# Kernel tuning notes

Hardware: AMD Instinct MI355X
Metric: run time of the kernel (lower is better)

Reference implementation:

```python
import jax, jax.numpy as jnp
import numpy as np

N = 100000      # nodes
E = 1600000     # edges (avg degree 16)
IN = 256        # in_dim
OUT = 64        # out_dim per head
H = 4           # num_heads
SLOPE = 0.01    # F.leaky_relu default negative_slope


def setup_inputs() -> dict:
    key = jax.random.key(0)
    k1, k2, k3, k4, k5 = jax.random.split(key, 5)
    h = jax.random.normal(k1, (N, IN), dtype=jnp.float32)
    # per-head projection Linear(in_dim, out_dim, bias=False): weight [OUT, IN]
    W = jax.random.normal(k2, (H, OUT, IN), dtype=jnp.float32) * (1.0 / np.sqrt(IN))
    # per-head attention Linear(2*out_dim, 1, bias=False): weight flattened to [2*OUT]
    attn = jax.random.normal(k3, (H, 2 * OUT), dtype=jnp.float32) * (1.0 / np.sqrt(2 * OUT))
    edge_src = jax.random.randint(k4, (E,), 0, N, dtype=jnp.int32)
    edge_dst = jax.random.randint(k5, (E,), 0, N, dtype=jnp.int32)
    return {"h": h, "W": W, "attn": attn, "edge_src": edge_src, "edge_dst": edge_dst}


def reference(h, W, attn, edge_src, edge_dst):
    # Bug-faithful: edge_attention always uses self.heads[0][1], i.e. head 0's
    # attention vector, for every head.
    a0 = attn[0]                      # [2*OUT]
    a_src, a_dst = a0[:OUT], a0[OUT:]
    outs = []
    for hd in range(H):               # fixed small structural loop over heads
        z = h @ W[hd].T               # [N, OUT]
        # concat(z_src, z_dst) @ a0 == z_src @ a_src + z_dst @ a_dst
        s_src = z @ a_src             # [N]
        s_dst = z @ a_dst             # [N]
        e = jax.nn.leaky_relu(s_src[edge_src] + s_dst[edge_dst], SLOPE)  # [E]
        # segment softmax over incoming edges of each destination node
        m = jax.ops.segment_max(e, edge_dst, num_segments=N)
        m = jnp.where(jnp.isfinite(m), m, 0.0)   # guard zero-in-degree nodes
        ex = jnp.exp(e - m[edge_dst])
        den = jax.ops.segment_sum(ex, edge_dst, num_segments=N)
        alpha = ex / jnp.maximum(den[edge_dst], 1e-9)          # [E]
        msg = alpha[:, None] * z[edge_src]                      # [E, OUT]
        outs.append(jax.ops.segment_sum(msg, edge_dst, num_segments=N))  # [N, OUT]
    return jnp.concatenate(outs, axis=1)  # merge='cat' -> [N, H*OUT]
```

## Files before the change

kernel.cpp:

```cpp
#include <hip/hip_runtime.h>

#define K_IN   256
#define C_OUT  256
#define HEADS  4
#define PAD    64
#define BKT    256
#define REP    16
#define CAP    448

typedef __attribute__((ext_vector_type(8))) short s16x8;
typedef __attribute__((ext_vector_type(4))) short s16x4;
typedef __attribute__((ext_vector_type(4))) float f32x4;
typedef __attribute__((ext_vector_type(4))) int   i32x4;

static __device__ __forceinline__ unsigned short f2bf(float f) {
  union { float f; unsigned u; } v; v.f = f;
  unsigned r = v.u + 0x7FFFu + ((v.u >> 16) & 1u);
  return (unsigned short)(r >> 16);
}
static __device__ __forceinline__ float bf2f(unsigned short u) {
  union { unsigned u; float f; } v; v.u = (unsigned)u << 16;
  return v.f;
}
static __device__ __forceinline__ unsigned cvt_pk_bf16(float lo, float hi) {
  unsigned r;
  asm volatile("v_cvt_pk_bf16_f32 %0, %1, %2" : "=v"(r) : "v"(lo), "v"(hi));
  return r;
}
static __device__ __forceinline__ float fast_exp2(float x) {
  float r;
  asm("v_exp_f32 %0, %1" : "=v"(r) : "v"(x));
  return r;
}

__global__ void cvt_w(const float* __restrict__ Wm, unsigned short* __restrict__ Wf) {
  int idx = blockIdx.x * blockDim.x + threadIdx.x;
  if (idx >= 65536) return;
  int j    = idx & 7;
  int lane = (idx >> 3) & 63;
  int s    = (idx >> 9) & 3;
  int ks   = (idx >> 11) & 7;
  int cb   = (idx >> 14) & 3;
  int c = cb * 64 + s * 16 + (lane & 15);
  int k = ks * 32 + (lane >> 4) * 8 + j;
  Wf[idx] = f2bf(Wm[c * K_IN + k]);
}

__global__ __launch_bounds__(256) void gemm_z(const float* __restrict__ h,
                                              const unsigned short* __restrict__ Wf,
                                              const float* __restrict__ attn,
                                              unsigned short* __restrict__ zb,
                                              float* __restrict__ ssrc,
                                              float* __restrict__ sdst, int n_nodes) {
  const int wv   = threadIdx.x >> 6;
  const int lane = threadIdx.x & 63;
  const int l15  = lane & 15;
  const int lhi  = lane >> 4;
  const int r0   = blockIdx.x * 64 + wv * 16;

  f32x4 acc[16];
#pragma unroll
  for (int f = 0; f < 16; ++f) acc[f] = (f32x4){0.f, 0.f, 0.f, 0.f};

  int n = r0 + l15;
  if (n > n_nodes - 1) n = n_nodes - 1;
  const long long arow = (long long)n * K_IN;
  const int kbase = lhi * 8;

#pragma unroll
  for (int ks = 0; ks < 8; ++ks) {
    const int k = ks * 32 + kbase;
    const float4* pa = reinterpret_cast<const float4*>(h + arow + k);
    float4 v0 = pa[0], v1 = pa[1];
    union { s16x8 v; unsigned u[4]; } au;
    au.u[0] = cvt_pk_bf16(v0.x, v0.y);
    au.u[1] = cvt_pk_bf16(v0.z, v0.w);
    au.u[2] = cvt_pk_bf16(v1.x, v1.y);
    au.u[3] = cvt_pk_bf16(v1.z, v1.w);
    s16x8 a = au.v;
#pragma unroll
    for (int f = 0; f < 16; ++f) {
      s16x8 b = *reinterpret_cast<const s16x8*>(
          Wf + (((f >> 2) * 8 + ks) * 4 + (f & 3)) * 512 + lane * 8);
      acc[f] = __builtin_amdgcn_mfma_f32_16x16x32_bf16(a, b, acc[f], 0, 0, 0);
    }
  }

#pragma unroll
  for (int reg = 0; reg < 4; ++reg) {
    int row = r0 + lhi * 4 + reg;
    if (row < n_nodes) {
#pragma unroll
      for (int f = 0; f < 16; ++f)
        zb[(size_t)row * C_OUT + f * 16 + l15] = f2bf(acc[f][reg]);
    }
  }

  const float LOG2E = 1.4426950408889634f;
  float as_[4], ad_[4];
#pragma unroll
  for (int s = 0; s < 4; ++s) {
    as_[s] = attn[s * 16 + l15];
    ad_[s] = attn[64 + s * 16 + l15];
  }
#pragma unroll
  for (int reg = 0; reg < 4; ++reg) {
    int row = r0 + lhi * 4 + reg;
    float ps[4], pd[4];
#pragma unroll
    for (int hd = 0; hd < 4; ++hd) {
      ps[hd] = acc[hd * 4 + 0][reg] * as_[0] + acc[hd * 4 + 1][reg] * as_[1] +
               acc[hd * 4 + 2][reg] * as_[2] + acc[hd * 4 + 3][reg] * as_[3];
      pd[hd] = acc[hd * 4 + 0][reg] * ad_[0] + acc[hd * 4 + 1][reg] * ad_[1] +
               acc[hd * 4 + 2][reg] * ad_[2] + acc[hd * 4 + 3][reg] * ad_[3];
#pragma unroll
      for (int d = 1; d < 16; d <<= 1) {
        ps[hd] += __shfl_xor(ps[hd], d, 64);
        pd[hd] += __shfl_xor(pd[hd], d, 64);
      }
    }
    if (l15 == 0 && row < n_nodes) {
#pragma unroll
      for (int hd = 0; hd < 4; ++hd) {
        ssrc[(size_t)row * 4 + hd] = ps[hd] * LOG2E;
        sdst[(size_t)row * 4 + hd] = pd[hd] * LOG2E;
      }
    }
  }
}

__global__ void scatter_r1(const int* __restrict__ src, const int* __restrict__ dst,
                           int E, int* __restrict__ cursors, int* __restrict__ stage) {
  int i = blockIdx.x * blockDim.x + threadIdx.x;
  int rep = blockIdx.x & (REP - 1);
  int e4 = E >> 2;
  if (i < e4) {
    i32x4 d = __builtin_nontemporal_load(reinterpret_cast<const i32x4*>(dst) + i);
    i32x4 s = __builtin_nontemporal_load(reinterpret_cast<const i32x4*>(src) + i);
#pragma unroll
    for (int k = 0; k < 4; ++k) {
      int c = (d[k] >> 8) * REP + rep;
      int p = atomicAdd(&cursors[c], 1);
      if (p < CAP) stage[c * CAP + p] = (s[k] << 8) | (d[k] & 255);
    }
  }
  if (i < (E & 3)) {
    int j = (e4 << 2) + i;
    int dd = dst[j], ss = src[j];
    int c = (dd >> 8) * REP + rep;
    int p = atomicAdd(&cursors[c], 1);
    if (p < CAP) stage[c * CAP + p] = (ss << 8) | (dd & 255);
  }
}

__global__ __launch_bounds__(256) void scatter_r2(const int* __restrict__ cursors,
                                                  const int* __restrict__ stage,
                                                  int N, int* __restrict__ counts,
                                                  int* __restrict__ csrp) {
  int b = blockIdx.x;
  int base = b << 8;
  __shared__ int cnt[BKT];
  for (int i = threadIdx.x; i < BKT; i += 256) cnt[i] = 0;
  __syncthreads();
  for (int rep = 0; rep < REP; ++rep) {
    int c = b * REP + rep;
    int len = min(cursors[c], CAP);
    for (int j = threadIdx.x; j < len; j += 256) {
      int v = stage[c * CAP + j];
      int d = v & 255, s = v >> 8;
      int slot = atomicAdd(&cnt[d], 1);
      if (slot < PAD) csrp[(size_t)(base + d) * PAD + slot] = s;
    }
  }
  __syncthreads();
  for (int i = threadIdx.x; i < BKT; i += 256) {
    int n = base + i;
    if (n < N) counts[n] = min(cnt[i], PAD);
  }
}

__global__ void scatter_pad(const int* __restrict__ src, const int* __restrict__ dst,
                            int e, int* __restrict__ cursor, int* __restrict__ csrp) {
  int i = blockIdx.x * blockDim.x + threadIdx.x;
  int e4 = e >> 2;
  if (i < e4) {
    i32x4 d = __builtin_nontemporal_load(reinterpret_cast<const i32x4*>(dst) + i);
    i32x4 s = __builtin_nontemporal_load(reinterpret_cast<const i32x4*>(src) + i);
#pragma unroll
    for (int k = 0; k < 4; ++k) {
      int p = atomicAdd(&cursor[d[k]], 1);
      csrp[d[k] * PAD + p] = s[k];
    }
  }
  if (i < (e & 3)) {
    int j = (e4 << 2) + i;
    int p = atomicAdd(&cursor[dst[j]], 1);
    csrp[dst[j] * PAD + p] = src[j];
  }
}

__global__ __launch_bounds__(256) void aggregate(const unsigned short* __restrict__ zb,
                                                 const float* __restrict__ ssrc,
                                                 const float* __restrict__ sdst,
                                                 const int* __restrict__ cnts,
                                                 const int* __restrict__ csr,
                                                 float* __restrict__ out,
                                                 int n0, int n1) {
  int w = n0 + blockIdx.x * (blockDim.x >> 6) + (threadIdx.x >> 6);
  if (w >= n1) return;
  int lane = threadIdx.x & 63;
  int head = lane >> 4;
  int beg = w * PAD;
  int end = beg + cnts[w];
  float sd = sdst[(size_t)w * 4 + head];
  float ax = 0.f, ay = 0.f, az = 0.f, aw = 0.f;
  float den = 0.f;
  for (int e = beg; e < end; e += 8) {
    int srcs[8];
#pragma unroll
    for (int j = 0; j < 8; ++j) {
      int idx = e + j;
      if (idx >= end) idx = end - 1;
      srcs[j] = __builtin_nontemporal_load(csr + idx);
    }
    float ss[8];
#pragma unroll
    for (int j = 0; j < 8; ++j)
      ss[j] = ssrc[(size_t)srcs[j] * 4 + head];
    s16x4 zv[8];
#pragma unroll
    for (int j = 0; j < 8; ++j)
      zv[j] = *reinterpret_cast<const s16x4*>(zb + (size_t)srcs[j] * C_OUT + lane * 4);
#pragma unroll
    for (int j = 0; j < 8; ++j) {
      float x = ss[j] + sd;
      x = x > 0.f ? x : 0.01f * x;
      float ex = fast_exp2(x);
      ex = (e + j < end) ? ex : 0.f;
      den += ex;
      ax += ex * bf2f((unsigned short)zv[j][0]);
      ay += ex * bf2f((unsigned short)zv[j][1]);
      az += ex * bf2f((unsigned short)zv[j][2]);
      aw += ex * bf2f((unsigned short)zv[j][3]);
    }
  }
  float inv = (end > beg) ? 1.f / fmaxf(den, 1e-9f) : 0.f;
  f32x4 o = {ax * inv, ay * inv, az * inv, aw * inv};
  __builtin_nontemporal_store(o, reinterpret_cast<f32x4*>(out + (size_t)w * C_OUT + lane * 4));
}

extern "C" void kernel_launch(void* const* d_in, const int* in_sizes, int n_in,
                              void* d_out, int out_size, void* d_ws, size_t ws_size,
                              hipStream_t stream) {
  const float* h    = (const float*)d_in[0];
  const float* Wm   = (const float*)d_in[1];
  const float* attn = (const float*)d_in[2];
  const int* e_src  = (const int*)d_in[3];
  const int* e_dst  = (const int*)d_in[4];
  float* out = (float*)d_out;

  const int N = in_sizes[0] / K_IN;
  const int E = in_sizes[3];
  const int NBK = (N + BKT - 1) / BKT;

  char* p = (char*)d_ws;
  unsigned short* zb = (unsigned short*)p; p += (size_t)N * C_OUT * sizeof(unsigned short);
  float* ssrc = (float*)p; p += (size_t)N * HEADS * sizeof(float);
  float* sdst = (float*)p; p += (size_t)N * HEADS * sizeof(float);
  int* counts = (int*)p;   p += (size_t)N * sizeof(int);
  unsigned short* Wf = (unsigned short*)p; p += 65536 * sizeof(unsigned short);
  int* csrp   = (int*)p;   p += (size_t)N * PAD * sizeof(int);
  int* cursors = (int*)p;  p += (size_t)NBK * REP * sizeof(int);
  int* stage   = (int*)p;
  const size_t need_binned = (size_t)(p - (char*)d_ws) + (size_t)NBK * REP * CAP * sizeof(int);
  const bool binned = ws_size >= need_binned;

  hipLaunchKernelGGL(cvt_w, dim3(256), dim3(256), 0, stream, Wm, Wf);

  hipLaunchKernelGGL(gemm_z, dim3((N + 63) / 64), dim3(256), 0, stream,
                     h, Wf, attn, zb, ssrc, sdst, N);

  if (binned) {
    (void)hipMemsetAsync(cursors, 0, (size_t)NBK * REP * sizeof(int), stream);
    hipLaunchKernelGGL(scatter_r1, dim3(((E >> 2) + 255) / 256), dim3(256), 0, stream,
                       e_src, e_dst, E, cursors, stage);
    hipLaunchKernelGGL(scatter_r2, dim3(NBK), dim3(256), 0, stream,
                       cursors, stage, N, counts, csrp);
  } else {
    (void)hipMemsetAsync(counts, 0, (size_t)N * sizeof(int), stream);
    hipLaunchKernelGGL(scatter_pad, dim3(((E >> 2) + 255) / 256), dim3(256), 0, stream,
                       e_src, e_dst, E, counts, csrp);
  }

  const int half = N / 2;
  hipLaunchKernelGGL(aggregate, dim3((half + 3) / 4), dim3(256), 0, stream,
                     zb, ssrc, sdst, counts, csrp, out, 0, half);
  hipLaunchKernelGGL(aggregate, dim3((N - half + 3) / 4), dim3(256), 0, stream,
                     zb, ssrc, sdst, counts, csrp, out, half, N);
}
```

Before: 312.2 us.

## Fuse projection GEMM and edge-binning scatter into one interleaved launch

The node projection GEMM and the first edge-binning scatter pass now run as a single kernel whose blocks alternate between the two roles. Compute-bound GEMM blocks and atomic-heavy scatter blocks can then share the GPU at the same time, and one launch is removed. In exchange the fused kernel takes on the GEMM's register pressure for every block, which can lower occupancy for the scatter blocks, and when the two grid sizes differ some blocks do no work.

```diff
diff --git a/kernel.cpp b/kernel.cpp
--- a/kernel.cpp
+++ b/kernel.cpp
@@ -46,17 +46,15 @@
   Wf[idx] = f2bf(Wm[c * K_IN + k]);
 }
 
-__global__ __launch_bounds__(256) void gemm_z(const float* __restrict__ h,
-                                              const unsigned short* __restrict__ Wf,
-                                              const float* __restrict__ attn,
-                                              unsigned short* __restrict__ zb,
-                                              float* __restrict__ ssrc,
-                                              float* __restrict__ sdst, int n_nodes) {
+static __device__ __forceinline__ void gemm_body(int bid,
+    const float* __restrict__ h, const unsigned short* __restrict__ Wf,
+    const float* __restrict__ attn, unsigned short* __restrict__ zb,
+    float* __restrict__ ssrc, float* __restrict__ sdst, int n_nodes) {
   const int wv   = threadIdx.x >> 6;
   const int lane = threadIdx.x & 63;
   const int l15  = lane & 15;
   const int lhi  = lane >> 4;
-  const int r0   = blockIdx.x * 64 + wv * 16;
+  const int r0   = bid * 64 + wv * 16;
 
   f32x4 acc[16];
 #pragma unroll
@@ -129,10 +127,11 @@
   }
 }
 
-__global__ void scatter_r1(const int* __restrict__ src, const int* __restrict__ dst,
-                           int E, int* __restrict__ cursors, int* __restrict__ stage) {
-  int i = blockIdx.x * blockDim.x + threadIdx.x;
-  int rep = blockIdx.x & (REP - 1);
+static __device__ __forceinline__ void scatter_body(int sbid,
+    const int* __restrict__ src, const int* __restrict__ dst, int E,
+    int* __restrict__ cursors, int* __restrict__ stage) {
+  int i = sbid * 256 + threadIdx.x;
+  int rep = sbid & (REP - 1);
   int e4 = E >> 2;
   if (i < e4) {
     i32x4 d = __builtin_nontemporal_load(reinterpret_cast<const i32x4*>(dst) + i);
@@ -150,6 +149,24 @@
     int c = (dd >> 8) * REP + rep;
     int p = atomicAdd(&cursors[c], 1);
     if (p < CAP) stage[c * CAP + p] = (ss << 8) | (dd & 255);
+  }
+}
+
+__global__ __launch_bounds__(256) void gemm_scatter(
+    const float* __restrict__ h, const unsigned short* __restrict__ Wf,
+    const float* __restrict__ attn, unsigned short* __restrict__ zb,
+    float* __restrict__ ssrc, float* __restrict__ sdst, int n_nodes,
+    int g_gemm, const int* __restrict__ e_src, const int* __restrict__ e_dst,
+    int E, int g_scat, int* __restrict__ cursors, int* __restrict__ stage) {
+  int bid = blockIdx.x;
+  if ((bid & 1) == 0) {
+    int g = bid >> 1;
+    if (g < g_gemm)
+      gemm_body(g, h, Wf, attn, zb, ssrc, sdst, n_nodes);
+  } else {
+    int s = bid >> 1;
+    if (s < g_scat)
+      scatter_body(s, e_src, e_dst, E, cursors, stage);
   }
 }
 
@@ -275,20 +292,25 @@
   const size_t need_binned = (size_t)(p - (char*)d_ws) + (size_t)NBK * REP * CAP * sizeof(int);
   const bool binned = ws_size >= need_binned;
 
+  const int g_gemm = (N + 63) / 64;
+  const int g_scat = ((E >> 2) + 255) / 256;
+
   hipLaunchKernelGGL(cvt_w, dim3(256), dim3(256), 0, stream, Wm, Wf);
-
-  hipLaunchKernelGGL(gemm_z, dim3((N + 63) / 64), dim3(256), 0, stream,
-                     h, Wf, attn, zb, ssrc, sdst, N);
 
   if (binned) {
     (void)hipMemsetAsync(cursors, 0, (size_t)NBK * REP * sizeof(int), stream);
-    hipLaunchKernelGGL(scatter_r1, dim3(((E >> 2) + 255) / 256), dim3(256), 0, stream,
-                       e_src, e_dst, E, cursors, stage);
+    const int gmax = (g_gemm > g_scat ? g_gemm : g_scat);
+    hipLaunchKernelGGL(gemm_scatter, dim3(2 * gmax), dim3(256), 0, stream,
+                       h, Wf, attn, zb, ssrc, sdst, N, g_gemm,
+                       e_src, e_dst, E, g_scat, cursors, stage);
     hipLaunchKernelGGL(scatter_r2, dim3(NBK), dim3(256), 0, stream,
                        cursors, stage, N, counts, csrp);
   } else {
+    hipLaunchKernelGGL(gemm_scatter, dim3(2 * g_gemm), dim3(256), 0, stream,
+                       h, Wf, attn, zb, ssrc, sdst, N, g_gemm,
+                       e_src, e_dst, 0, 0, (int*)nullptr, (int*)nullptr);
     (void)hipMemsetAsync(counts, 0, (size_t)N * sizeof(int), stream);
-    hipLaunchKernelGGL(scatter_pad, dim3(((E >> 2) + 255) / 256), dim3(256), 0, stream,
+    hipLaunchKernelGGL(scatter_pad, dim3(g_scat), dim3(256), 0, stream,
                        e_src, e_dst, E, counts, csrp);
   }
 
```

After: 271.1 us. 13.2% less time.
